# Kernel optimization log

Hardware: AMD Instinct MI355X
Metric: run time of the kernel (lower is better)

## Reference

```python
import jax, jax.numpy as jnp
import numpy as np

# Config constants (match init_kwargs)
H = 1024   # hidden_size
F = 4096   # intermediate_size
E = 8      # num_moe_experts
K = 2      # moe_router_topk
S, B = 1024, 2  # seq_len, micro-batch


def setup_inputs() -> dict:
    key = jax.random.key(0)
    ks = jax.random.split(key, 6)
    return {
        "hidden_states": jax.random.normal(ks[0], (S, B, H), jnp.float32),
        "router_w": jax.random.normal(ks[1], (H, E), jnp.float32) * 0.02,
        "w1": jax.random.normal(ks[2], (E, H, F), jnp.float32) * 0.02,
        "b1": jax.random.normal(ks[3], (E, F), jnp.float32) * 0.02,
        "w2": jax.random.normal(ks[4], (E, F, H), jnp.float32) * 0.02,
        "b2": jax.random.normal(ks[5], (E, H), jnp.float32) * 0.02,
    }


def reference(hidden_states, router_w, w1, b1, w2, b2):
    S_, B_, H_ = hidden_states.shape
    x = hidden_states.reshape(-1, H_)                      # [N, H]
    N = x.shape[0]

    # --- TopKRouter (aux_loss routing): topk over logits, softmax over top-k logits ---
    logits = x @ router_w                                  # [N, E]
    top_logits, indices = jax.lax.top_k(logits, K)         # [N, K]
    scores = jax.nn.softmax(top_logits.astype(jnp.float32), axis=-1).astype(logits.dtype)

    # Combine weights [N, E]: scatter top-k scores into expert slots.
    combine = jnp.zeros((N, E), x.dtype).at[jnp.arange(N)[:, None], indices].add(scores)

    # --- Experts: per-expert GPTNeoXMLP (dense over all tokens; math-equivalent
    # to dispatch (token_permutation) + grouped GEMM + scatter_add combine
    # (token_unpermutation) with score weighting for topk>1) ---
    h = jax.nn.gelu(jnp.einsum('nh,ehf->enf', x, w1) + b1[:, None, :], approximate=False)
    y = jnp.einsum('enf,efh->enh', h, w2) + b2[:, None, :]  # [E, N, H]

    out = jnp.einsum('ne,enh->nh', combine, y)              # weighted combine
    return out.reshape(S_, B_, H_)
```

## Files before the change

kernel.cpp:

```cpp
#include <hip/hip_runtime.h>
#include <cmath>


#define H_DIM 1024
#define F_DIM 4096
#define E_NUM 8
#define N_TOK 2048
#define BK 32
#define MAX_SLOTS 5120
#define MAX_MT 40
#define G1_GRID (MAX_MT * 32)
#define G2_GRID (MAX_MT * 8 * 2)
#define XCHUNKS (N_TOK * H_DIM / 8)

typedef short s16x4 __attribute__((ext_vector_type(4)));
typedef short s16x8 __attribute__((ext_vector_type(8)));
typedef float f32x4 __attribute__((ext_vector_type(4)));
typedef __attribute__((address_space(3))) const unsigned short* lds_us;

__device__ __forceinline__ unsigned short f2bf(float f) {
  unsigned int u = __float_as_uint(f);
  u += 0x7fffu + ((u >> 16) & 1u);
  return (unsigned short)(u >> 16);
}

__device__ __forceinline__ void gload_lds16(const void* g, void* l) {
  __builtin_amdgcn_global_load_lds(
      (const __attribute__((address_space(1))) unsigned int*)g,
      (__attribute__((address_space(3))) unsigned int*)l, 16, 0, 0);
}

__device__ __forceinline__ float fast_gelu(float v) {
  const float w = v * (1.0f + 0.044715f * v * v);
  const float t = __expf(-1.5957691216f * w);
  return v / (1.0f + t);
}

__device__ __forceinline__ unsigned int pk_bf16(float lo, float hi) {
  unsigned int r;
  asm("v_cvt_pk_bf16_f32 %0, %1, %2" : "=v"(r) : "v"(lo), "v"(hi));
  return r;
}

template<int OFS>
__device__ __forceinline__ s16x4 trread(lds_us p) {
  s16x4 r;
  asm volatile("ds_read_b64_tr_b16 %0, %1 offset:%2" : "=v"(r) : "v"(p), "i"(OFS));
  return r;
}

__device__ __forceinline__ void ld_b4(lds_us bp, s16x8 bb[4]) {
  s16x4 p0 = trread<0>(bp),    q0 = trread<512>(bp);
  s16x4 p1 = trread<1040>(bp), q1 = trread<1552>(bp);
  s16x4 p2 = trread<2080>(bp), q2 = trread<2592>(bp);
  s16x4 p3 = trread<3120>(bp), q3 = trread<3632>(bp);
  bb[0] = __builtin_shufflevector(p0, q0, 0, 1, 2, 3, 4, 5, 6, 7);
  bb[1] = __builtin_shufflevector(p1, q1, 0, 1, 2, 3, 4, 5, 6, 7);
  bb[2] = __builtin_shufflevector(p2, q2, 0, 1, 2, 3, 4, 5, 6, 7);
  bb[3] = __builtin_shufflevector(p3, q3, 0, 1, 2, 3, 4, 5, 6, 7);
}

__global__ __launch_bounds__(256) void prep_k(
    const float* __restrict__ x, unsigned short* __restrict__ xb,
    const float* __restrict__ rw, int* __restrict__ topk_e, float* __restrict__ topk_s) {
  const int b = blockIdx.x;
  const int t = threadIdx.x;
  if (b < 128) {
    const int step = 128 * 256;
#pragma unroll 4
    for (int c = b * 256 + t; c < XCHUNKS; c += step) {
      const size_t i = (size_t)c * 8;
      f32x4 a = *(const f32x4*)(x + i);
      f32x4 d = *(const f32x4*)(x + i + 4);
      s16x8 u;
#pragma unroll
      for (int j = 0; j < 4; ++j) { u[j] = (short)f2bf(a[j]); u[4 + j] = (short)f2bf(d[j]); }
      *(s16x8*)&xb[i] = u;
    }
    return;
  }
  const int n = (b - 128) * 4 + (t >> 6);
  const int l = t & 63;
  float part[E_NUM];
#pragma unroll
  for (int e = 0; e < E_NUM; ++e) part[e] = 0.f;
  const float* xr = x + (size_t)n * H_DIM;
  for (int h = l; h < H_DIM; h += 64) {
    const float xv = xr[h];
    const float* rwr = rw + h * E_NUM;
#pragma unroll
    for (int e = 0; e < E_NUM; ++e) part[e] += xv * rwr[e];
  }
#pragma unroll
  for (int e = 0; e < E_NUM; ++e) {
#pragma unroll
    for (int off = 32; off > 0; off >>= 1) part[e] += __shfl_down(part[e], off);
  }
  if (l == 0) {
    float v0 = -3.4e38f, v1 = -3.4e38f;
    int i0 = 0, i1 = 0;
#pragma unroll
    for (int e = 0; e < E_NUM; ++e) {
      float v = part[e];
      if (v > v0) { v1 = v0; i1 = i0; v0 = v; i0 = e; }
      else if (v > v1) { v1 = v; i1 = e; }
    }
    const float e1 = expf(v1 - v0);
    const float inv = 1.f / (1.f + e1);
    topk_e[2 * n] = i0; topk_e[2 * n + 1] = i1;
    topk_s[2 * n] = inv; topk_s[2 * n + 1] = e1 * inv;
  }
}

__global__ __launch_bounds__(256) void scatter_k(
    int* __restrict__ meta, const int* __restrict__ topk_e,
    int* __restrict__ slot_token, int* __restrict__ token_slots) {
  __shared__ int cnt[4][8];
  __shared__ int soff[9];
  __shared__ int scur[8];
  const int t = threadIdx.x;
  const int wv = t >> 6;
  if (t < 32) cnt[t >> 3][t & 7] = 0;
  if (t < 8) scur[t] = 0;
  __syncthreads();
  for (int a = t; a < N_TOK * 2; a += 256)
    atomicAdd(&cnt[wv][topk_e[a]], 1);
  __syncthreads();
  if (t == 0) {
    int acc = 0;
    for (int e = 0; e < E_NUM; ++e) {
      const int c = cnt[0][e] + cnt[1][e] + cnt[2][e] + cnt[3][e];
      soff[e] = acc;
      meta[8 + e] = acc;
      acc += ((c + 127) / 128) * 128;
    }
    soff[8] = acc;
    meta[16] = acc;
  }
  __syncthreads();
  for (int a = t; a < N_TOK * 2; a += 256) {
    const int e = topk_e[a];
    const int pos = atomicAdd(&scur[e], 1);
    const int slot = soff[e] + pos;
    slot_token[slot] = a >> 1;
    token_slots[a] = slot;
  }
}

__global__ __launch_bounds__(256, 3) void gemm1_f(
    const unsigned short* __restrict__ xb, const float* __restrict__ w1,
    const float* __restrict__ b1, const int* __restrict__ meta,
    const int* __restrict__ slot_token, unsigned short* __restrict__ hbuf) {
  __shared__ __align__(16) unsigned short Al[3 * 4096];
  __shared__ __align__(16) char Bl[2 * 8 * 1040];
  const int total = meta[16];
  const int c = blockIdx.x & 7;
  const int j = blockIdx.x >> 3;
  const int mt = j >> 2, nt = c * 4 + (j & 3);
  const int m0 = mt * 128;
  if (m0 >= total) return;
  int exp = 0;
#pragma unroll
  for (int e = 1; e < E_NUM; ++e) if (m0 >= meta[8 + e]) exp = e;
  const int n0 = nt * 128;
  const int t = threadIdx.x, w = t >> 6, l = t & 63;
  const int wm = w >> 1, wn = w & 1, lr = l & 15, lg = l >> 4;

  const unsigned short* pA[2];
#pragma unroll
  for (int i = 0; i < 2; ++i) {
    const int q = w * 2 + i;
    const int row = q * 16 + (l >> 2);
    int tk = slot_token[m0 + row]; if (tk < 0) tk = 0;
    pA[i] = xb + (size_t)tk * H_DIM + (((l & 3) ^ ((l >> 3) & 3)) << 3);
  }
  const int krow = t >> 3, cg = t & 7;
  const float* pB = w1 + (size_t)exp * H_DIM * F_DIM + (size_t)krow * F_DIM + n0 + cg * 16;
  const int wb = cg * 1040 + ((krow >> 2) & 1) * 512 + (krow >> 3) * 128 + (krow & 3) * 32;

  const f32x4 fzero = {0.f, 0.f, 0.f, 0.f};
  f32x4 acc[4][4];
#pragma unroll
  for (int a = 0; a < 4; ++a)
#pragma unroll
    for (int b = 0; b < 4; ++b) acc[a][b] = fzero;
  const int fofs = ((lg ^ ((lr >> 1) & 3)) << 3);

#define ISSUEA1(Ad)                                                         \
  _Pragma("unroll") for (int i = 0; i < 2; ++i) {                           \
    gload_lds16(pA[i], (Ad) + (w * 2 + i) * 512); pA[i] += BK;              \
  }
#define LOADB1(v)                                                           \
  { _Pragma("unroll") for (int q_ = 0; q_ < 4; ++q_) v[q_] = *(const f32x4*)(pB + q_ * 4); \
    pB += (size_t)BK * F_DIM; }
#define CVTB1(v, Bd)                                                        \
  { int4 u0, u1;                                                            \
    u0.x = (int)pk_bf16(v[0][0], v[0][1]); u0.y = (int)pk_bf16(v[0][2], v[0][3]); \
    u0.z = (int)pk_bf16(v[1][0], v[1][1]); u0.w = (int)pk_bf16(v[1][2], v[1][3]); \
    u1.x = (int)pk_bf16(v[2][0], v[2][1]); u1.y = (int)pk_bf16(v[2][2], v[2][3]); \
    u1.z = (int)pk_bf16(v[3][0], v[3][1]); u1.w = (int)pk_bf16(v[3][2], v[3][3]); \
    *(int4*)((Bd) + wb) = u0; *(int4*)((Bd) + wb + 16) = u1; }
#define MFMA1(Ac, Bc)                                                       \
  { lds_us bp = (lds_us)((Bc) + wn * 4160) + l * 4;                         \
    s16x8 af[4], bb[4];                                                     \
    _Pragma("unroll") for (int fm = 0; fm < 4; ++fm)                        \
      af[fm] = *(const s16x8*)&(Ac)[(wm * 64 + fm * 16 + lr) * 32 + fofs];  \
    ld_b4(bp, bb);                                                          \
    asm volatile("s_waitcnt lgkmcnt(0)" ::: "memory");                      \
    __builtin_amdgcn_sched_barrier(0);                                      \
    _Pragma("unroll") for (int fm = 0; fm < 4; ++fm)                        \
      _Pragma("unroll") for (int fn = 0; fn < 4; ++fn)                      \
        acc[fm][fn] = __builtin_amdgcn_mfma_f32_16x16x32_bf16(af[fm], bb[fn], acc[fm][fn], 0, 0, 0); \
  }

  unsigned short *a0 = Al, *a1 = Al + 4096, *a2 = Al + 8192;
  char *bl0 = Bl, *bl1 = Bl + 8320;
  f32x4 vP[4], vQ[4];
  const int NT = H_DIM / BK;
  LOADB1(vP) ISSUEA1(a0)
  LOADB1(vQ) ISSUEA1(a1)
  asm volatile("s_waitcnt vmcnt(6)" ::: "memory");
  CVTB1(vP, bl0)
  asm volatile("s_waitcnt lgkmcnt(0)" ::: "memory");
  __builtin_amdgcn_s_barrier();
  for (int it = 0; it < NT / 2; ++it) {
    const bool has2 = it < NT / 2 - 1;
    if (has2) { ISSUEA1(a2) LOADB1(vP) }
    if (has2) asm volatile("s_waitcnt vmcnt(6)" ::: "memory");
    else      asm volatile("s_waitcnt vmcnt(0)" ::: "memory");
    CVTB1(vQ, bl1)
    MFMA1(a0, bl0)
    asm volatile("s_waitcnt lgkmcnt(0)" ::: "memory");
    __builtin_amdgcn_s_barrier();
    { unsigned short* tmp = a0; a0 = a1; a1 = a2; a2 = tmp; }
    if (has2) { ISSUEA1(a2) LOADB1(vQ) }
    if (has2) asm volatile("s_waitcnt vmcnt(6)" ::: "memory");
    else      asm volatile("s_waitcnt vmcnt(0)" ::: "memory");
    if (has2) { CVTB1(vP, bl0) }
    MFMA1(a0, bl1)
    if (has2) {
      asm volatile("s_waitcnt lgkmcnt(0)" ::: "memory");
      __builtin_amdgcn_s_barrier();
    }
    { unsigned short* tmp = a0; a0 = a1; a1 = a2; a2 = tmp; }
  }

#pragma unroll
  for (int fn = 0; fn < 4; ++fn) {
    const int col = n0 + wn * 64 + fn * 16 + lr;
    const float bias = b1[exp * F_DIM + col];
#pragma unroll
    for (int fm = 0; fm < 4; ++fm) {
      const int rbase = m0 + wm * 64 + fm * 16 + lg * 4;
#pragma unroll
      for (int i = 0; i < 4; ++i) {
        hbuf[(size_t)(rbase + i) * F_DIM + col] = f2bf(fast_gelu(acc[fm][fn][i] + bias));
      }
    }
  }
}

__global__ __launch_bounds__(256, 3) void gemm2_f(
    const unsigned short* __restrict__ hbuf, const float* __restrict__ w2,
    const int* __restrict__ meta, unsigned short* __restrict__ yb) {
  __shared__ __align__(16) unsigned short Al[3 * 4096];
  __shared__ __align__(16) char Bl[2 * 8 * 1040];
  const int total = meta[16];
  const int c = blockIdx.x & 7;
  const int r = blockIdx.x >> 3;
  const int nt = c;
  const int ks = r & 1;
  const int mt = r >> 1;
  const int m0 = mt * 128;
  if (m0 >= total) return;
  int exp = 0;
#pragma unroll
  for (int e = 1; e < E_NUM; ++e) if (m0 >= meta[8 + e]) exp = e;
  const int n0 = nt * 128;
  const int k0 = ks * 2048;
  const int t = threadIdx.x, w = t >> 6, l = t & 63;
  const int wm = w >> 1, wn = w & 1, lr = l & 15, lg = l >> 4;

  const unsigned short* pA[2];
#pragma unroll
  for (int i = 0; i < 2; ++i) {
    const int q = w * 2 + i;
    const int row = q * 16 + (l >> 2);
    pA[i] = hbuf + (size_t)(m0 + row) * F_DIM + k0 + (((l & 3) ^ ((l >> 3) & 3)) << 3);
  }
  const int krow = t >> 3, cg = t & 7;
  const float* pB = w2 + (size_t)exp * F_DIM * H_DIM + (size_t)(k0 + krow) * H_DIM + n0 + cg * 16;
  const int wb = cg * 1040 + ((krow >> 2) & 1) * 512 + (krow >> 3) * 128 + (krow & 3) * 32;

  const f32x4 fzero = {0.f, 0.f, 0.f, 0.f};
  f32x4 acc[4][4];
#pragma unroll
  for (int a = 0; a < 4; ++a)
#pragma unroll
    for (int b = 0; b < 4; ++b) acc[a][b] = fzero;
  const int fofs = ((lg ^ ((lr >> 1) & 3)) << 3);

#define ISSUEA2(Ad)                                                         \
  _Pragma("unroll") for (int i = 0; i < 2; ++i) {                           \
    gload_lds16(pA[i], (Ad) + (w * 2 + i) * 512); pA[i] += BK;              \
  }
#define LOADB2(v)                                                           \
  { _Pragma("unroll") for (int q_ = 0; q_ < 4; ++q_) v[q_] = *(const f32x4*)(pB + q_ * 4); \
    pB += (size_t)BK * H_DIM; }

  unsigned short *a0 = Al, *a1 = Al + 4096, *a2 = Al + 8192;
  char *bl0 = Bl, *bl1 = Bl + 8320;
  f32x4 vP[4], vQ[4];
  const int NT = 2048 / BK;
  LOADB2(vP) ISSUEA2(a0)
  LOADB2(vQ) ISSUEA2(a1)
  asm volatile("s_waitcnt vmcnt(6)" ::: "memory");
  CVTB1(vP, bl0)
  asm volatile("s_waitcnt lgkmcnt(0)" ::: "memory");
  __builtin_amdgcn_s_barrier();
  for (int it = 0; it < NT / 2; ++it) {
    const bool has2 = it < NT / 2 - 1;
    if (has2) { ISSUEA2(a2) LOADB2(vP) }
    if (has2) asm volatile("s_waitcnt vmcnt(6)" ::: "memory");
    else      asm volatile("s_waitcnt vmcnt(0)" ::: "memory");
    CVTB1(vQ, bl1)
    MFMA1(a0, bl0)
    asm volatile("s_waitcnt lgkmcnt(0)" ::: "memory");
    __builtin_amdgcn_s_barrier();
    { unsigned short* tmp = a0; a0 = a1; a1 = a2; a2 = tmp; }
    if (has2) { ISSUEA2(a2) LOADB2(vQ) }
    if (has2) asm volatile("s_waitcnt vmcnt(6)" ::: "memory");
    else      asm volatile("s_waitcnt vmcnt(0)" ::: "memory");
    if (has2) { CVTB1(vP, bl0) }
    MFMA1(a0, bl1)
    if (has2) {
      asm volatile("s_waitcnt lgkmcnt(0)" ::: "memory");
      __builtin_amdgcn_s_barrier();
    }
    { unsigned short* tmp = a0; a0 = a1; a1 = a2; a2 = tmp; }
  }

  unsigned short* yk = yb + (size_t)ks * MAX_SLOTS * H_DIM;
#pragma unroll
  for (int fn = 0; fn < 4; ++fn) {
    const int col = n0 + wn * 64 + fn * 16 + lr;
#pragma unroll
    for (int fm = 0; fm < 4; ++fm) {
      const int rbase = m0 + wm * 64 + fm * 16 + lg * 4;
#pragma unroll
      for (int i = 0; i < 4; ++i) {
        yk[(size_t)(rbase + i) * H_DIM + col] = f2bf(acc[fm][fn][i]);
      }
    }
  }
}

__global__ __launch_bounds__(256) void combine_k(
    const unsigned short* __restrict__ yb, const float* __restrict__ b2,
    const int* __restrict__ token_slots, const int* __restrict__ topk_e,
    const float* __restrict__ topk_s, float* __restrict__ out) {
  const int tok = blockIdx.x;
  const int c4 = threadIdx.x * 4;
  const int sl0 = token_slots[2 * tok], sl1 = token_slots[2 * tok + 1];
  const float s0 = topk_s[2 * tok], s1 = topk_s[2 * tok + 1];
  const int e0 = topk_e[2 * tok], e1 = topk_e[2 * tok + 1];
  const unsigned short* y1p = yb + (size_t)MAX_SLOTS * H_DIM;
  ushort4 a0 = *(const ushort4*)(yb  + (size_t)sl0 * H_DIM + c4);
  ushort4 a1 = *(const ushort4*)(y1p + (size_t)sl0 * H_DIM + c4);
  ushort4 d0 = *(const ushort4*)(yb  + (size_t)sl1 * H_DIM + c4);
  ushort4 d1 = *(const ushort4*)(y1p + (size_t)sl1 * H_DIM + c4);
  f32x4 ba = *(const f32x4*)(b2 + e0 * H_DIM + c4);
  f32x4 bd = *(const f32x4*)(b2 + e1 * H_DIM + c4);
  const unsigned short* ap0 = &a0.x; const unsigned short* ap1 = &a1.x;
  const unsigned short* dp0 = &d0.x; const unsigned short* dp1 = &d1.x;
  f32x4 o;
#pragma unroll
  for (int j = 0; j < 4; ++j) {
    const float ya = __uint_as_float((unsigned)ap0[j] << 16) + __uint_as_float((unsigned)ap1[j] << 16) + ba[j];
    const float yd = __uint_as_float((unsigned)dp0[j] << 16) + __uint_as_float((unsigned)dp1[j] << 16) + bd[j];
    o[j] = s0 * ya + s1 * yd;
  }
  *(f32x4*)(out + (size_t)tok * H_DIM + c4) = o;
}

extern "C" void kernel_launch(void* const* d_in, const int* in_sizes, int n_in,
                              void* d_out, int out_size, void* d_ws, size_t ws_size,
                              hipStream_t stream) {
  const float* x  = (const float*)d_in[0];
  const float* rw = (const float*)d_in[1];
  const float* w1 = (const float*)d_in[2];
  const float* b1 = (const float*)d_in[3];
  const float* w2 = (const float*)d_in[4];
  const float* b2 = (const float*)d_in[5];
  float* out = (float*)d_out;
  char* ws = (char*)d_ws;

  int*   meta        = (int*)ws;
  int*   topk_e      = (int*)(ws + 4096);
  float* topk_s      = (float*)(ws + 36864);
  int*   slot_token  = (int*)(ws + 69632);
  int*   token_slots = (int*)(ws + 102400);
  unsigned short* xb   = (unsigned short*)(ws + (1ull << 20));
  unsigned short* hbuf = (unsigned short*)(ws + (6ull << 20));
  unsigned short* yb   = (unsigned short*)(ws + (46ull << 20));

  hipMemsetAsync(meta, 0, 256, stream);
  hipMemsetAsync(slot_token, 0xFF, MAX_SLOTS * sizeof(int), stream);

  prep_k<<<128 + 512, 256, 0, stream>>>(x, xb, rw, topk_e, topk_s);
  scatter_k<<<1, 256, 0, stream>>>(meta, topk_e, slot_token, token_slots);
  gemm1_f<<<G1_GRID, 256, 0, stream>>>(xb, w1, b1, meta, slot_token, hbuf);
  gemm2_f<<<G2_GRID, 256, 0, stream>>>(hbuf, w2, meta, yb);
  combine_k<<<N_TOK, 256, 0, stream>>>(yb, b2, token_slots, topk_e, topk_s, out);
}
```

Before: 227.9 us.

## Deepen B-operand register prefetch in GEMM2 to four-stage rotation

The second expert GEMM now keeps four register buffers of fp32 B tiles in flight instead of two. Global loads for B are issued two iterations ahead, with retuned vmcnt waits and an explicit prologue and epilogue. The loop is unrolled by four so the register rotation stays static. The aim is to hide global-load latency for the fp32 weight stream, at the cost of more VGPRs and possibly lower occupancy.

```diff
diff --git a/kernel.cpp b/kernel.cpp
--- a/kernel.cpp
+++ b/kernel.cpp
@@ -310,35 +310,53 @@
 
   unsigned short *a0 = Al, *a1 = Al + 4096, *a2 = Al + 8192;
   char *bl0 = Bl, *bl1 = Bl + 8320;
-  f32x4 vP[4], vQ[4];
+  f32x4 v0[4], v1[4], v2[4], v3[4];
   const int NT = 2048 / BK;
-  LOADB2(vP) ISSUEA2(a0)
-  LOADB2(vQ) ISSUEA2(a1)
-  asm volatile("s_waitcnt vmcnt(6)" ::: "memory");
-  CVTB1(vP, bl0)
+
+  ISSUEA2(a0) LOADB2(v0)
+  ISSUEA2(a1) LOADB2(v1)
+  LOADB2(v2)
+  asm volatile("s_waitcnt vmcnt(10)" ::: "memory");
+  CVTB1(v0, bl0)
   asm volatile("s_waitcnt lgkmcnt(0)" ::: "memory");
   __builtin_amdgcn_s_barrier();
-  for (int it = 0; it < NT / 2; ++it) {
-    const bool has2 = it < NT / 2 - 1;
-    if (has2) { ISSUEA2(a2) LOADB2(vP) }
-    if (has2) asm volatile("s_waitcnt vmcnt(6)" ::: "memory");
-    else      asm volatile("s_waitcnt vmcnt(0)" ::: "memory");
-    CVTB1(vQ, bl1)
-    MFMA1(a0, bl0)
-    asm volatile("s_waitcnt lgkmcnt(0)" ::: "memory");
+
+#define STEP2(VL, VC, BLW, BLR)                                             \
+  {                                                                         \
+    ISSUEA2(a2) LOADB2(VL)                                                  \
+    asm volatile("s_waitcnt vmcnt(12)" ::: "memory");                       \
+    CVTB1(VC, BLW)                                                          \
+    MFMA1(a0, BLR)                                                          \
+    asm volatile("s_waitcnt vmcnt(10) lgkmcnt(0)" ::: "memory");            \
+    __builtin_amdgcn_s_barrier();                                           \
+    { unsigned short* tmp = a0; a0 = a1; a1 = a2; a2 = tmp; }               \
+  }
+
+  for (int it = 0; it < (NT - 4) / 4; ++it) {
+    STEP2(v3, v1, bl1, bl0)
+    STEP2(v0, v2, bl0, bl1)
+    STEP2(v1, v3, bl1, bl0)
+    STEP2(v2, v0, bl0, bl1)
+  }
+  STEP2(v3, v1, bl1, bl0)
+  {
+    ISSUEA2(a2)
+    asm volatile("s_waitcnt vmcnt(8)" ::: "memory");
+    CVTB1(v2, bl0)
+    MFMA1(a0, bl1)
+    asm volatile("s_waitcnt vmcnt(6) lgkmcnt(0)" ::: "memory");
     __builtin_amdgcn_s_barrier();
     { unsigned short* tmp = a0; a0 = a1; a1 = a2; a2 = tmp; }
-    if (has2) { ISSUEA2(a2) LOADB2(vQ) }
-    if (has2) asm volatile("s_waitcnt vmcnt(6)" ::: "memory");
-    else      asm volatile("s_waitcnt vmcnt(0)" ::: "memory");
-    if (has2) { CVTB1(vP, bl0) }
-    MFMA1(a0, bl1)
-    if (has2) {
-      asm volatile("s_waitcnt lgkmcnt(0)" ::: "memory");
-      __builtin_amdgcn_s_barrier();
-    }
+  }
+  {
+    asm volatile("s_waitcnt vmcnt(2)" ::: "memory");
+    CVTB1(v3, bl1)
+    MFMA1(a0, bl0)
+    asm volatile("s_waitcnt vmcnt(0) lgkmcnt(0)" ::: "memory");
+    __builtin_amdgcn_s_barrier();
     { unsigned short* tmp = a0; a0 = a1; a1 = a2; a2 = tmp; }
   }
+  MFMA1(a0, bl1)
 
   unsigned short* yk = yb + (size_t)ks * MAX_SLOTS * H_DIM;
 #pragma unroll
```

Result: slower. 300.2 us (+31.7%).
